# Optimization experiments

Measured on AMD Instinct MI355X. Metric: run time of the kernel, lower is better.

## Reference

```python
import jax, jax.numpy as jnp
import numpy as np

B, N, IN_DIM, HID = 8, 2048, 128, 64
LN_EPS = 1e-5
NEG_INF = -9e15
LRELU_SLOPE = 0.2


def setup_inputs() -> dict:
    key = jax.random.key(0)
    k1, k2, k3, k4, k5, k6 = jax.random.split(key, 6)
    stdv = 1.0 / np.sqrt(HID)
    adj = jax.random.randint(k1, (B, N, N), 0, 2, dtype=jnp.int32)
    # ensure self-loops so every row has at least one valid entry
    adj = adj.at[:, jnp.arange(N), jnp.arange(N)].set(1)
    return {
        "adj": adj,
        "x": jax.random.normal(k2, (B, N, IN_DIM), dtype=jnp.float32),
        "h": jax.random.normal(k3, (B, N, HID), dtype=jnp.float32),
        "X2H": jax.random.uniform(k4, (IN_DIM, 3 * HID), minval=-stdv, maxval=stdv, dtype=jnp.float32),
        "H2H": jax.random.uniform(k5, (HID, 3 * HID), minval=-stdv, maxval=stdv, dtype=jnp.float32),
        "a": jax.random.uniform(k6, (2 * HID, 1), minval=-stdv, maxval=stdv, dtype=jnp.float32),
    }


def _gated_inputs(x, h, X2H, H2H):
    gate_x = x @ X2H          # [B,N,3H]
    gate_h = h @ H2H          # [B,N,3H]
    i_r, i_i, i_n = jnp.split(gate_x, 3, axis=2)
    h_r, h_i, h_n = jnp.split(gate_h, 3, axis=2)
    resetgate = jax.nn.sigmoid(i_r + h_r)
    inputgate = jax.nn.sigmoid(i_i + h_i)
    irh = i_n + resetgate * h_n
    mu = jnp.mean(irh, axis=-1, keepdims=True)
    var = jnp.mean(jnp.square(irh - mu), axis=-1, keepdims=True)
    irh = (irh - mu) * jax.lax.rsqrt(var + LN_EPS)  # layer_norm, no affine
    newgate = jnp.tanh(irh)
    return newgate + inputgate * (h - newgate)


def reference(adj, x, h, X2H, H2H, a):
    Wh = _gated_inputs(x, h, X2H, H2H)              # [B,N,H]
    Wh1 = Wh @ a[:HID]                              # [B,N,1]
    Wh2 = Wh @ a[HID:]                              # [B,N,1]
    e = jax.nn.leaky_relu(Wh1 + jnp.swapaxes(Wh2, 1, 2), LRELU_SLOPE)  # [B,N,N]
    scores = jnp.where(adj != 0, e, jnp.float32(NEG_INF))
    attention = jax.nn.softmax(scores, axis=2)
    h_prime = attention @ Wh                        # [B,N,H]
    return (h_prime, Wh)
```

## Files before the change

kernel.cpp:

```cpp
#include <hip/hip_runtime.h>

constexpr int BB  = 8;
constexpr int NN  = 2048;
constexpr int IND = 128;
constexpr int HD  = 64;
constexpr float LN_EPS = 1e-5f;
constexpr float SLOPE  = 0.2f;

typedef _Float16 half8 __attribute__((ext_vector_type(8)));
typedef _Float16 half4 __attribute__((ext_vector_type(4)));
typedef float    f32x4 __attribute__((ext_vector_type(4)));

__device__ __forceinline__ float wave_sum(float v) {
    #pragma unroll
    for (int off = 32; off > 0; off >>= 1) v += __shfl_xor(v, off);
    return v;
}
__device__ __forceinline__ float wave_max(float v) {
    #pragma unroll
    for (int off = 32; off > 0; off >>= 1) v = fmaxf(v, __shfl_xor(v, off));
    return v;
}

__global__ void k_prep(const float* __restrict__ X2H, const float* __restrict__ H2H,
                       _Float16* __restrict__ Wt)
{
    const int tot = 256 * 192;
    for (int idx = blockIdx.x * 256 + threadIdx.x; idx < tot; idx += gridDim.x * 256) {
        const int col = idx / 192, k = idx % 192;
        float v;
        if (col < 128)       v = (k < 128) ? X2H[(size_t)k * 192 + col]
                                           : H2H[(size_t)(k - 128) * 192 + col];
        else if (col < 192)  v = (k < 128) ? X2H[(size_t)k * 192 + col] : 0.f;
        else                 v = (k >= 128) ? H2H[(size_t)(k - 128) * 192 + (col - 64)] : 0.f;
        Wt[idx] = (_Float16)v;
    }
}

__global__ __launch_bounds__(256, 4) void k_gates(
    const float* __restrict__ x, const float* __restrict__ h,
    const _Float16* __restrict__ Wt, const float* __restrict__ a,
    float* __restrict__ Wh_out, _Float16* __restrict__ Whh2,
    float* __restrict__ Wh1, float* __restrict__ Wh2)
{
    __shared__ float gbuf[16][260];

    const int tid = threadIdx.x, lane = tid & 63, w = tid >> 6;
    const int m = lane & 15, q = lane >> 4;
    const int row0 = blockIdx.x * 16;

    f32x4 acc[4];
    #pragma unroll
    for (int ct = 0; ct < 4; ++ct) acc[ct] = (f32x4){0.f, 0.f, 0.f, 0.f};

    #pragma unroll
    for (int kc = 0; kc < 6; ++kc) {
        half8 a8;
        if (kc < 4) {
            const float* xp = x + (size_t)(row0 + m) * IND + kc * 32 + q * 8;
            const f32x4 v0 = *(const f32x4*)xp;
            const f32x4 v1 = *(const f32x4*)(xp + 4);
            #pragma unroll
            for (int j = 0; j < 4; ++j) { a8[j] = (_Float16)v0[j]; a8[4 + j] = (_Float16)v1[j]; }
        } else {
            const float* hp_ = h + (size_t)(row0 + m) * HD + (kc - 4) * 32 + q * 8;
            const f32x4 v0 = *(const f32x4*)hp_;
            const f32x4 v1 = *(const f32x4*)(hp_ + 4);
            #pragma unroll
            for (int j = 0; j < 4; ++j) { a8[j] = (_Float16)v0[j]; a8[4 + j] = (_Float16)v1[j]; }
        }
        #pragma unroll
        for (int ct = 0; ct < 4; ++ct) {
            const half8 b8 = *(const half8*)(Wt + ((size_t)(w * 64 + ct * 16 + m) * 192 + kc * 32 + q * 8));
            acc[ct] = __builtin_amdgcn_mfma_f32_16x16x32_f16(a8, b8, acc[ct], 0, 0, 0);
        }
    }

    #pragma unroll
    for (int ct = 0; ct < 4; ++ct)
        #pragma unroll
        for (int r2 = 0; r2 < 4; ++r2)
            gbuf[q * 4 + r2][w * 64 + ct * 16 + m] = acc[ct][r2];
    __syncthreads();

    const float a0 = a[lane], a1 = a[64 + lane];
    half4 p4;
    const int grow0 = row0 + w * 4;
    #pragma unroll
    for (int r = 0; r < 4; ++r) {
        const int row = w * 4 + r;
        const int grow = row0 + row;
        const float g0 = gbuf[row][lane];
        const float g1 = gbuf[row][64 + lane];
        const float g2 = gbuf[row][128 + lane];
        const float g3 = gbuf[row][192 + lane];
        const float rg = 1.f / (1.f + __expf(-g0));
        const float ig = 1.f / (1.f + __expf(-g1));
        const float irh = g2 + rg * g3;
        const float mu = wave_sum(irh) * (1.f / 64.f);
        const float dv = irh - mu;
        const float var = wave_sum(dv * dv) * (1.f / 64.f);
        const float ng = tanhf(dv * rsqrtf(var + LN_EPS));
        const float hr = h[(size_t)grow * HD + lane];
        const float wh = ng + ig * (hr - ng);
        Wh_out[(size_t)grow * HD + lane] = wh;
        p4[r] = (_Float16)wh;
        const float d1 = wave_sum(wh * a0);
        const float d2 = wave_sum(wh * a1);
        if (lane == 0) { Wh1[grow] = d1; Wh2[grow] = d2; }
    }
    *(half4*)(Whh2 + ((size_t)(grow0 >> 3) * 64 + lane) * 8 + (w & 1) * 4) = p4;
}

constexpr int KC  = 256;
constexpr int PST = KC + 8;

__global__ __launch_bounds__(256, 3) void k_attn(
    const int* __restrict__ adj,
    const _Float16* __restrict__ Whh2,
    const float* __restrict__ Wh1, const float* __restrict__ Wh2,
    float* __restrict__ hp)
{
    __shared__ __align__(16) char smem[4 * 16 * PST * 2];
    __shared__ float ssum[4][16];
    __shared__ float redb[4];

    const int tid  = threadIdx.x;
    const int lane = tid & 63;
    const int w    = tid >> 6;
    const int b    = blockIdx.x >> 7;
    const int i0   = (blockIdx.x & 127) * 16;
    const int m    = lane & 15;
    const int q    = lane >> 4;

    _Float16* __restrict__ Pw = (_Float16*)smem + w * 16 * PST;

    const f32x4* __restrict__ w2v = (const f32x4*)(Wh2 + (size_t)b * NN);
    f32x4 wv[2];
    #pragma unroll
    for (int t = 0; t < 2; ++t) wv[t] = w2v[(2 * w + t) * 64 + lane];

    float mx = fmaxf(fmaxf(wv[0][0], wv[0][1]), fmaxf(wv[0][2], wv[0][3]));
    mx = fmaxf(mx, fmaxf(fmaxf(wv[1][0], wv[1][1]), fmaxf(wv[1][2], wv[1][3])));
    mx = wave_max(mx);
    if (lane == 0) redb[w] = mx;
    __syncthreads();
    const float M = fmaxf(fmaxf(redb[0], redb[1]), fmaxf(redb[2], redb[3]));

    float w1r[16], cr[16];
    #pragma unroll
    for (int r = 0; r < 16; ++r) {
        w1r[r] = Wh1[b * NN + i0 + r];
        const float t0 = w1r[r] + M;
        cr[r] = (t0 > 0.f) ? t0 : SLOPE * t0;
    }

    const int* __restrict__ abase = adj + ((size_t)b * NN + i0) * NN;
    const half8* __restrict__ Wp = (const half8*)(Whh2 + (size_t)b * NN * HD);

    float sacc[16];
    #pragma unroll
    for (int r = 0; r < 16; ++r) sacc[r] = 0.f;
    f32x4 acc[4];
    #pragma unroll
    for (int cc = 0; cc < 4; ++cc) acc[cc] = (f32x4){0.f, 0.f, 0.f, 0.f};

    int4 av[16];
    #pragma unroll
    for (int r = 0; r < 16; ++r)
        av[r] = *(const int4*)(abase + (size_t)r * NN + (2 * w) * KC + 4 * lane);

    #pragma unroll
    for (int t = 0; t < 2; ++t) {
        const int c = 2 * w + t;
        #pragma unroll
        for (int r = 0; r < 16; ++r) {
            const int ai[4] = {av[r].x, av[r].y, av[r].z, av[r].w};
            half4 ph;
            float s = 0.f;
            #pragma unroll
            for (int d = 0; d < 4; ++d) {
                const float tt = w1r[r] + wv[t][d];
                const float e = (tt > 0.f) ? tt : SLOPE * tt;
                const float p = ai[d] ? __expf(e - cr[r]) : 0.f;
                s += p;
                ph[d] = (_Float16)p;
            }
            sacc[r] += s;
            *(half4*)&Pw[r * PST + 4 * lane] = ph;
        }
        if (t == 0) {
            #pragma unroll
            for (int r = 0; r < 16; ++r)
                av[r] = *(const int4*)(abase + (size_t)r * NN + (2 * w + 1) * KC + 4 * lane);
        }
        __syncthreads();

        #pragma unroll
        for (int k8 = 0; k8 < 8; ++k8) {
            const half8 a8 = *(const half8*)&Pw[m * PST + k8 * 32 + q * 8];
            #pragma unroll
            for (int cc = 0; cc < 4; ++cc) {
                const half8 b8 = Wp[(size_t)(c * 32 + k8 * 4 + q) * 64 + cc * 16 + m];
                acc[cc] = __builtin_amdgcn_mfma_f32_16x16x32_f16(a8, b8, acc[cc], 0, 0, 0);
            }
        }
        __syncthreads();
    }

    #pragma unroll
    for (int r = 0; r < 16; ++r) {
        const float s = wave_sum(sacc[r]);
        if (lane == 0) ssum[w][r] = s;
    }
    float* __restrict__ accb = (float*)smem;
    #pragma unroll
    for (int cc = 0; cc < 4; ++cc)
        *(f32x4*)&accb[((w * 64 + lane) * 4 + cc) * 4] = acc[cc];
    __syncthreads();

    f32x4 tot = (f32x4){0.f, 0.f, 0.f, 0.f};
    #pragma unroll
    for (int wp = 0; wp < 4; ++wp) {
        const f32x4 t4 = *(const f32x4*)&accb[((wp * 64 + lane) * 4 + w) * 4];
        tot[0] += t4[0]; tot[1] += t4[1]; tot[2] += t4[2]; tot[3] += t4[3];
    }
    #pragma unroll
    for (int r2 = 0; r2 < 4; ++r2) {
        const int irow = q * 4 + r2;
        const float S = ssum[0][irow] + ssum[1][irow] + ssum[2][irow] + ssum[3][irow];
        hp[((size_t)b * NN + i0 + irow) * HD + w * 16 + m] = tot[r2] / S;
    }
}

extern "C" void kernel_launch(void* const* d_in, const int* in_sizes, int n_in,
                              void* d_out, int out_size, void* d_ws, size_t ws_size,
                              hipStream_t stream) {
    const int*   adj = (const int*)d_in[0];
    const float* x   = (const float*)d_in[1];
    const float* h   = (const float*)d_in[2];
    const float* X2H = (const float*)d_in[3];
    const float* H2H = (const float*)d_in[4];
    const float* a   = (const float*)d_in[5];

    float* out = (float*)d_out;
    float* hp  = out;
    float* Wh  = out + (size_t)BB * NN * HD;

    float*    Wh1  = (float*)d_ws;
    float*    Wh2  = Wh1 + BB * NN;
    _Float16* Whh2 = (_Float16*)(Wh2 + BB * NN);
    _Float16* Wt   = Whh2 + (size_t)BB * NN * HD;

    k_prep<<<dim3(64), dim3(256), 0, stream>>>(X2H, H2H, Wt);
    k_gates<<<dim3((BB * NN) / 16), dim3(256), 0, stream>>>(
        x, h, Wt, a, Wh, Whh2, Wh1, Wh2);
    k_attn<<<dim3(BB * (NN / 16)), dim3(256), 0, stream>>>(
        adj, Whh2, Wh1, Wh2, hp);
}
```

Before: 289.1 us.

## Split attention block across 8 waves, one key chunk each, with pipelined adj loads

The attention kernel now runs 512 threads (8 waves) per 16-row block, with each wave owning a single 256-column chunk instead of two. Adjacency rows are loaded in groups of four with double buffering rather than all 16 rows at once, which lowers register pressure and allows more waves in flight. Per-row sums are reduced per wave immediately, and the final cross-wave accumulation uses a padded shared-memory stride. This trades more shared memory and a wider cross-wave reduction for more memory-level parallelism on the adjacency stream.

```diff
diff --git a/kernel.cpp b/kernel.cpp
--- a/kernel.cpp
+++ b/kernel.cpp
@@ -115,15 +115,15 @@
 constexpr int KC  = 256;
 constexpr int PST = KC + 8;
 
-__global__ __launch_bounds__(256, 3) void k_attn(
+__global__ __launch_bounds__(512, 4) void k_attn(
     const int* __restrict__ adj,
     const _Float16* __restrict__ Whh2,
     const float* __restrict__ Wh1, const float* __restrict__ Wh2,
     float* __restrict__ hp)
 {
-    __shared__ __align__(16) char smem[4 * 16 * PST * 2];
-    __shared__ float ssum[4][16];
-    __shared__ float redb[4];
+    __shared__ __align__(16) _Float16 Pall[8 * 16 * PST];
+    __shared__ float ssum[8][16];
+    __shared__ float redb[8];
 
     const int tid  = threadIdx.x;
     const int lane = tid & 63;
@@ -133,103 +133,100 @@
     const int m    = lane & 15;
     const int q    = lane >> 4;
 
-    _Float16* __restrict__ Pw = (_Float16*)smem + w * 16 * PST;
-
-    const f32x4* __restrict__ w2v = (const f32x4*)(Wh2 + (size_t)b * NN);
-    f32x4 wv[2];
-    #pragma unroll
-    for (int t = 0; t < 2; ++t) wv[t] = w2v[(2 * w + t) * 64 + lane];
-
-    float mx = fmaxf(fmaxf(wv[0][0], wv[0][1]), fmaxf(wv[0][2], wv[0][3]));
-    mx = fmaxf(mx, fmaxf(fmaxf(wv[1][0], wv[1][1]), fmaxf(wv[1][2], wv[1][3])));
+    _Float16* __restrict__ Pw = Pall + w * 16 * PST;
+
+    const f32x4 wv = ((const f32x4*)(Wh2 + (size_t)b * NN))[w * 64 + lane];
+
+    float mx = fmaxf(fmaxf(wv[0], wv[1]), fmaxf(wv[2], wv[3]));
     mx = wave_max(mx);
     if (lane == 0) redb[w] = mx;
     __syncthreads();
-    const float M = fmaxf(fmaxf(redb[0], redb[1]), fmaxf(redb[2], redb[3]));
-
-    float w1r[16], cr[16];
-    #pragma unroll
-    for (int r = 0; r < 16; ++r) {
-        w1r[r] = Wh1[b * NN + i0 + r];
-        const float t0 = w1r[r] + M;
-        cr[r] = (t0 > 0.f) ? t0 : SLOPE * t0;
-    }
-
-    const int* __restrict__ abase = adj + ((size_t)b * NN + i0) * NN;
-    const half8* __restrict__ Wp = (const half8*)(Whh2 + (size_t)b * NN * HD);
-
-    float sacc[16];
-    #pragma unroll
-    for (int r = 0; r < 16; ++r) sacc[r] = 0.f;
-    f32x4 acc[4];
-    #pragma unroll
-    for (int cc = 0; cc < 4; ++cc) acc[cc] = (f32x4){0.f, 0.f, 0.f, 0.f};
-
-    int4 av[16];
-    #pragma unroll
-    for (int r = 0; r < 16; ++r)
-        av[r] = *(const int4*)(abase + (size_t)r * NN + (2 * w) * KC + 4 * lane);
-
-    #pragma unroll
-    for (int t = 0; t < 2; ++t) {
-        const int c = 2 * w + t;
-        #pragma unroll
-        for (int r = 0; r < 16; ++r) {
-            const int ai[4] = {av[r].x, av[r].y, av[r].z, av[r].w};
+    float M = redb[0];
+    #pragma unroll
+    for (int i = 1; i < 8; ++i) M = fmaxf(M, redb[i]);
+
+    float w1r[16];
+    #pragma unroll
+    for (int r = 0; r < 16; ++r) w1r[r] = Wh1[b * NN + i0 + r];
+
+    const int* __restrict__ abase = adj + ((size_t)b * NN + i0) * NN + w * KC + 4 * lane;
+
+    int4 buf0[4], buf1[4];
+    #pragma unroll
+    for (int r = 0; r < 4; ++r) buf0[r] = *(const int4*)(abase + (size_t)r * NN);
+    #pragma unroll
+    for (int r = 0; r < 4; ++r) buf1[r] = *(const int4*)(abase + (size_t)(4 + r) * NN);
+
+    #pragma unroll
+    for (int g = 0; g < 4; ++g) {
+        #pragma unroll
+        for (int rr = 0; rr < 4; ++rr) {
+            const int r = g * 4 + rr;
+            const int4 av = (g & 1) ? buf1[rr] : buf0[rr];
+            const int ai[4] = {av.x, av.y, av.z, av.w};
+            const float t0 = w1r[r] + M;
+            const float c  = (t0 > 0.f) ? t0 : SLOPE * t0;
             half4 ph;
             float s = 0.f;
             #pragma unroll
             for (int d = 0; d < 4; ++d) {
-                const float tt = w1r[r] + wv[t][d];
-                const float e = (tt > 0.f) ? tt : SLOPE * tt;
-                const float p = ai[d] ? __expf(e - cr[r]) : 0.f;
+                const float t = w1r[r] + wv[d];
+                const float e = (t > 0.f) ? t : SLOPE * t;
+                const float p = ai[d] ? __expf(e - c) : 0.f;
                 s += p;
                 ph[d] = (_Float16)p;
             }
-            sacc[r] += s;
+            s = wave_sum(s);
+            if (lane == 0) ssum[w][r] = s;
             *(half4*)&Pw[r * PST + 4 * lane] = ph;
         }
-        if (t == 0) {
-            #pragma unroll
-            for (int r = 0; r < 16; ++r)
-                av[r] = *(const int4*)(abase + (size_t)r * NN + (2 * w + 1) * KC + 4 * lane);
-        }
-        __syncthreads();
-
-        #pragma unroll
-        for (int k8 = 0; k8 < 8; ++k8) {
-            const half8 a8 = *(const half8*)&Pw[m * PST + k8 * 32 + q * 8];
-            #pragma unroll
-            for (int cc = 0; cc < 4; ++cc) {
-                const half8 b8 = Wp[(size_t)(c * 32 + k8 * 4 + q) * 64 + cc * 16 + m];
-                acc[cc] = __builtin_amdgcn_mfma_f32_16x16x32_f16(a8, b8, acc[cc], 0, 0, 0);
+        if (g + 2 < 4) {
+            #pragma unroll
+            for (int rr = 0; rr < 4; ++rr) {
+                int4 nv = *(const int4*)(abase + (size_t)((g + 2) * 4 + rr) * NN);
+                if (g & 1) buf1[rr] = nv; else buf0[rr] = nv;
             }
         }
-        __syncthreads();
-    }
-
-    #pragma unroll
-    for (int r = 0; r < 16; ++r) {
-        const float s = wave_sum(sacc[r]);
-        if (lane == 0) ssum[w][r] = s;
-    }
-    float* __restrict__ accb = (float*)smem;
+    }
+    __syncthreads();
+
+    const half8* __restrict__ Wp = (const half8*)(Whh2 + (size_t)b * NN * HD);
+    f32x4 acc[4];
+    #pragma unroll
+    for (int cc = 0; cc < 4; ++cc) acc[cc] = (f32x4){0.f, 0.f, 0.f, 0.f};
+
+    #pragma unroll
+    for (int k8 = 0; k8 < 8; ++k8) {
+        const half8 a8 = *(const half8*)&Pw[m * PST + k8 * 32 + q * 8];
+        #pragma unroll
+        for (int cc = 0; cc < 4; ++cc) {
+            const half8 b8 = Wp[(size_t)(w * 32 + k8 * 4 + q) * 64 + cc * 16 + m];
+            acc[cc] = __builtin_amdgcn_mfma_f32_16x16x32_f16(a8, b8, acc[cc], 0, 0, 0);
+        }
+    }
+    __syncthreads();
+
+    float* __restrict__ accb = (float*)Pall;
     #pragma unroll
     for (int cc = 0; cc < 4; ++cc)
-        *(f32x4*)&accb[((w * 64 + lane) * 4 + cc) * 4] = acc[cc];
-    __syncthreads();
-
-    f32x4 tot = (f32x4){0.f, 0.f, 0.f, 0.f};
-    #pragma unroll
-    for (int wp = 0; wp < 4; ++wp) {
-        const f32x4 t4 = *(const f32x4*)&accb[((wp * 64 + lane) * 4 + w) * 4];
-        tot[0] += t4[0]; tot[1] += t4[1]; tot[2] += t4[2]; tot[3] += t4[3];
-    }
-    #pragma unroll
-    for (int r2 = 0; r2 < 4; ++r2) {
-        const int irow = q * 4 + r2;
-        const float S = ssum[0][irow] + ssum[1][irow] + ssum[2][irow] + ssum[3][irow];
-        hp[((size_t)b * NN + i0 + irow) * HD + w * 16 + m] = tot[r2] / S;
+        *(f32x4*)&accb[(w * 64 + lane) * 17 + cc * 4] = acc[cc];
+    __syncthreads();
+
+    if (w < 4) {
+        f32x4 tot = (f32x4){0.f, 0.f, 0.f, 0.f};
+        #pragma unroll
+        for (int wp = 0; wp < 8; ++wp) {
+            const f32x4 t4 = *(const f32x4*)&accb[(wp * 64 + lane) * 17 + w * 4];
+            tot[0] += t4[0]; tot[1] += t4[1]; tot[2] += t4[2]; tot[3] += t4[3];
+        }
+        #pragma unroll
+        for (int r2 = 0; r2 < 4; ++r2) {
+            const int irow = q * 4 + r2;
+            float S = 0.f;
+            #pragma unroll
+            for (int wp = 0; wp < 8; ++wp) S += ssum[wp][irow];
+            hp[((size_t)b * NN + i0 + irow) * HD + w * 16 + m] = tot[r2] / S;
+        }
     }
 }
 
@@ -255,6 +252,6 @@
     k_prep<<<dim3(64), dim3(256), 0, stream>>>(X2H, H2H, Wt);
     k_gates<<<dim3((BB * NN) / 16), dim3(256), 0, stream>>>(
         x, h, Wt, a, Wh, Whh2, Wh1, Wh2);
-    k_attn<<<dim3(BB * (NN / 16)), dim3(256), 0, stream>>>(
+    k_attn<<<dim3(BB * (NN / 16)), dim3(512), 0, stream>>>(
         adj, Whh2, Wh1, Wh2, hp);
 }
```

After: 239.3 us. 1.21x faster.
